# Performance work log

Measured on AMD Instinct MI355X. Metric: run time of the kernel, lower is better.

## Reference

```python
import jax, jax.numpy as jnp
import numpy as np
import math

VOCAB = 32000
D_MODEL = 512
N_LAYERS = 6
N_HEADS = 8
DIM_FF = 2048
B, L = 4, 2048
MAX_LEN = 5000
EPS = 1e-5


def _pos_encoding(max_len, d_model):
    pe = np.zeros((max_len, d_model), dtype=np.float32)
    pos = np.arange(max_len)[:, None].astype(np.float32)
    div = np.exp(np.arange(0, d_model, 2).astype(np.float32) * (-math.log(10000.0) / d_model))
    pe[:, 0::2] = np.sin(pos * div)
    pe[:, 1::2] = np.cos(pos * div)
    return jnp.asarray(pe)


def setup_inputs() -> dict:
    key = jax.random.key(0)
    ks = jax.random.split(key, 16)
    s = 0.02
    d, f, Ly = D_MODEL, DIM_FF, N_LAYERS
    inp = {
        "src": jax.random.randint(ks[0], (B, L), 0, VOCAB, dtype=jnp.int32),
        "embed": jax.random.normal(ks[1], (VOCAB, d), jnp.float32) * s,
        "pe": _pos_encoding(MAX_LEN, d),
        "Wq": jax.random.normal(ks[2], (Ly, d, d), jnp.float32) * s,
        "bq": jnp.zeros((Ly, d), jnp.float32),
        "Wk": jax.random.normal(ks[3], (Ly, d, d), jnp.float32) * s,
        "bk": jnp.zeros((Ly, d), jnp.float32),
        "Wv": jax.random.normal(ks[4], (Ly, d, d), jnp.float32) * s,
        "bv": jnp.zeros((Ly, d), jnp.float32),
        "Wo": jax.random.normal(ks[5], (Ly, d, d), jnp.float32) * s,
        "bo": jnp.zeros((Ly, d), jnp.float32),
        "W1": jax.random.normal(ks[6], (Ly, d, f), jnp.float32) * s,
        "b1": jnp.zeros((Ly, f), jnp.float32),
        "W2": jax.random.normal(ks[7], (Ly, f, d), jnp.float32) * s,
        "b2": jnp.zeros((Ly, d), jnp.float32),
        "g1": jnp.ones((Ly, d), jnp.float32),
        "be1": jnp.zeros((Ly, d), jnp.float32),
        "g2": jnp.ones((Ly, d), jnp.float32),
        "be2": jnp.zeros((Ly, d), jnp.float32),
    }
    return inp


def _layernorm(x, g, b):
    mu = jnp.mean(x, axis=-1, keepdims=True)
    var = jnp.mean((x - mu) ** 2, axis=-1, keepdims=True)
    return (x - mu) * jax.lax.rsqrt(var + EPS) * g + b


def _encoder(src, embed, pe, Wq, bq, Wk, bk, Wv, bv, Wo, bo, W1, b1, W2, b2, g1, be1, g2, be2):
    Bb, Ll = src.shape
    H = N_HEADS
    hd = D_MODEL // H
    x = embed[src] + pe[:Ll]  # [B, L, D]
    for i in range(Wq.shape[0]):
        # NOTE: faithful to the source: .view(B, H, L, hd) with NO transpose
        q = (x @ Wq[i] + bq[i]).reshape(Bb, H, Ll, hd)
        k = (x @ Wk[i] + bk[i]).reshape(Bb, H, Ll, hd)
        v = (x @ Wv[i] + bv[i]).reshape(Bb, H, Ll, hd)
        scores = jnp.einsum('bhqd,bhkd->bhqk', q, k) / math.sqrt(hd)
        w = jax.nn.softmax(scores, axis=-1)
        o = jnp.einsum('bhqk,bhkd->bhqd', w, v)
        o = o.transpose(0, 2, 1, 3).reshape(Bb, Ll, D_MODEL)
        o = o @ Wo[i] + bo[i]
        x = _layernorm(x + o, g1[i], be1[i])
        ff = jax.nn.relu(x @ W1[i] + b1[i]) @ W2[i] + b2[i]
        x = _layernorm(x + ff, g2[i], be2[i])
    return x


def reference(src, embed, pe, Wq, bq, Wk, bk, Wv, bv, Wo, bo, W1, b1, W2, b2, g1, be1, g2, be2):
    return _encoder(src, embed, pe, Wq, bq, Wk, bk, Wv, bv, Wo, bo, W1, b1, W2, b2, g1, be1, g2, be2)
```

## Files before the change

### kernel.cpp

```cpp
#include <hip/hip_runtime.h>
#include <hip/hip_bf16.h>

typedef unsigned short u16;
typedef __attribute__((ext_vector_type(8))) short bf16x8;
typedef __attribute__((ext_vector_type(2))) unsigned u32x2;
typedef __attribute__((ext_vector_type(4))) float f32x4;

#define B_  4
#define L_  2048
#define D_  512
#define H_  8
#define HD_ 64
#define FF_ 2048
#define NL_ 6
#define M_  8192
#define MB_ 1048576ULL

#if __has_builtin(__builtin_amdgcn_exp2f)
#define EX2 __builtin_amdgcn_exp2f
#else
#define EX2 exp2f
#endif

__device__ __forceinline__ float b2f(u16 u) {
    unsigned v = ((unsigned)u) << 16;
    return __builtin_bit_cast(float, v);
}
__device__ __forceinline__ u16 f2b(float f) {
    unsigned u = __builtin_bit_cast(unsigned, f);
    unsigned r = u + 0x7FFFu + ((u >> 16) & 1u);
    return (u16)(r >> 16);
}
__device__ __forceinline__ unsigned pack2_bf16(float a, float b) {
    __hip_bfloat162 h = __float22bfloat162_rn(make_float2(a, b));
    unsigned u;
    __builtin_memcpy(&u, &h, 4);
    return u;
}
__device__ __forceinline__ float inp(const void* p, size_t i, int fp32) {
    return fp32 ? ((const float*)p)[i] : b2f(((const u16*)p)[i]);
}
__device__ __forceinline__ void gl2lds16(const void* g, void* l) {
    __builtin_amdgcn_global_load_lds(
        (const __attribute__((address_space(1))) void*)g,
        (__attribute__((address_space(3))) void*)l, 16, 0, 0);
}

__global__ void probe_k(const unsigned* __restrict__ g1, int* __restrict__ flag) {
    flag[0] = (g1[0] == 0x3F800000u) ? 1 : 0;
}

__global__ __launch_bounds__(256) void transpose_layer_k2(const void* __restrict__ Wq,
                                                          const void* __restrict__ Wk,
                                                          const void* __restrict__ Wv,
                                                          const void* __restrict__ Wo,
                                                          const void* __restrict__ W1,
                                                          const void* __restrict__ W2,
                                                          size_t wo, size_t wf,
                                                          u16* __restrict__ Wt,
                                                          const int* __restrict__ flag) {
    __shared__ u16 tile[32][33];
    int fp32 = flag[0];
    int bid = blockIdx.x;
    const void* in;
    size_t off;
    u16* out;
    int rows, cols, tx, ty;
    if (bid < 1024) {
        int which = bid >> 8;
        in = (which == 0) ? Wq : (which == 1) ? Wk : (which == 2) ? Wv : Wo;
        off = wo;
        out = Wt + (size_t)which * (512 * 512);
        rows = 512; cols = 512;
        int t = bid & 255; tx = t & 15; ty = t >> 4;
    } else if (bid < 2048) {
        in = W1; off = wf; out = Wt + 4 * (512 * 512);
        rows = 512; cols = 2048;
        int t = bid - 1024; tx = t & 63; ty = t >> 6;
    } else {
        in = W2; off = wf; out = Wt + 4 * (512 * 512) + 512 * 2048;
        rows = 2048; cols = 512;
        int t = bid - 2048; tx = t & 15; ty = t >> 4;
    }
    int c0 = tx * 32, r0 = ty * 32;
    int lx = threadIdx.x & 31, ly = threadIdx.x >> 5;
    #pragma unroll
    for (int i = ly; i < 32; i += 8)
        tile[i][lx] = f2b(inp(in, off + (size_t)(r0 + i) * cols + c0 + lx, fp32));
    __syncthreads();
    #pragma unroll
    for (int i = ly; i < 32; i += 8)
        out[(size_t)(c0 + i) * rows + r0 + lx] = tile[lx][i];
}

__global__ __launch_bounds__(256) void embed_k(const int* __restrict__ src,
                                               const void* __restrict__ embed,
                                               const void* __restrict__ pe,
                                               float* __restrict__ xf,
                                               u16* __restrict__ xb,
                                               const int* __restrict__ flag) {
    int fp32 = flag[0];
    int idx = blockIdx.x * 256 + threadIdx.x;
    int m = idx >> 9;
    int d = idx & 511;
    int tok = src[m];
    float v = inp(embed, (size_t)tok * D_ + d, fp32)
            + inp(pe, (size_t)(m & (L_ - 1)) * D_ + d, fp32);
    xf[idx] = v;
    xb[idx] = f2b(v);
}

template <int TM, int TN, int WM, int WN, int WRITE_BF16, int RELU>
__device__ __forceinline__ void gemm_core(const u16* __restrict__ A,
                                          const u16* __restrict__ Bt,
                                          int tnB, int tnC,
                                          const void* __restrict__ bias, size_t boff,
                                          float* __restrict__ Cf, u16* __restrict__ Cb,
                                          int N, int K, int kbeg, int kend,
                                          float cscale, int fp32, int use_bias) {
    constexpr int BK = 32;
    __shared__ u16 Asm[TM * BK];
    __shared__ u16 Bsm[TN * BK];
    int tm = blockIdx.y * TM;
    int tid = threadIdx.x;
    int wave = tid >> 6, lane = tid & 63, quad = lane >> 4, l16 = lane & 15;
    constexpr int NWN = TN / WN;
    int wm = (wave / NWN) * WM, wn = (wave % NWN) * WN;
    constexpr int FI = WM / 16, FJ = WN / 16;
    constexpr int CA = TM / 64;
    constexpr int CB = TN / 64;

    int arowl = (lane >> 2);
    int akc   = (lane & 3) * 8;

    f32x4 acc[FI][FJ];
    #pragma unroll
    for (int i = 0; i < FI; i++)
        #pragma unroll
        for (int j = 0; j < FJ; j++) { f32x4 z = {0.f, 0.f, 0.f, 0.f}; acc[i][j] = z; }

    for (int k0 = kbeg; k0 < kend; k0 += BK) {
        __syncthreads();
        #pragma unroll
        for (int c = 0; c < CA; c++) {
            int chunk = wave * CA + c;
            int row = chunk * 16 + arowl;
            gl2lds16(A + (size_t)(tm + row) * K + k0 + akc, &Asm[chunk * 16 * BK]);
        }
        #pragma unroll
        for (int c = 0; c < CB; c++) {
            int chunk = wave * CB + c;
            int row = chunk * 16 + arowl;
            gl2lds16(Bt + (size_t)(tnB + row) * K + k0 + akc, &Bsm[chunk * 16 * BK]);
        }
        __syncthreads();
        bf16x8 af[FI], bfr[FJ];
        #pragma unroll
        for (int i = 0; i < FI; i++)
            af[i] = *(bf16x8*)&Asm[(wm + i * 16 + l16) * BK + quad * 8];
        #pragma unroll
        for (int j = 0; j < FJ; j++)
            bfr[j] = *(bf16x8*)&Bsm[(wn + j * 16 + l16) * BK + quad * 8];
        #pragma unroll
        for (int i = 0; i < FI; i++)
            #pragma unroll
            for (int j = 0; j < FJ; j++)
                acc[i][j] = __builtin_amdgcn_mfma_f32_16x16x32_bf16(af[i], bfr[j], acc[i][j], 0, 0, 0);
    }

    #pragma unroll
    for (int i = 0; i < FI; i++) {
        int row = tm + wm + i * 16 + quad * 4;
        #pragma unroll
        for (int j = 0; j < FJ; j++) {
            int col = tnC + wn + j * 16 + l16;
            float bv = use_bias ? inp(bias, boff + col, fp32) : 0.f;
            #pragma unroll
            for (int r = 0; r < 4; r++) {
                float v = (acc[i][j][r] + bv) * cscale;
                if (RELU) v = v > 0.f ? v : 0.f;
                size_t idx = (size_t)(row + r) * N + col;
                if (WRITE_BF16) Cb[idx] = f2b(v);
                else            Cf[idx] = v;
            }
        }
    }
}

__global__ __launch_bounds__(256) void gemm_qkv(const u16* A, const u16* Wt,
                                                const void* bq, const void* bk, const void* bv,
                                                size_t boff, u16* Qb, u16* Kb, u16* Vb,
                                                int K, float qscale, const int* flag) {
    int tnB = blockIdx.x * 128;
    int mat = tnB >> 9;
    int tnC = tnB & 511;
    u16* Cb = (mat == 0) ? Qb : (mat == 1) ? Kb : Vb;
    const void* bias = (mat == 0) ? bq : (mat == 1) ? bk : bv;
    float sc = (mat == 0) ? qscale : 1.0f;
    gemm_core<128, 128, 64, 64, 1, 0>(A, Wt, tnB, tnC, bias, boff, nullptr, Cb, 512, K, 0, K, sc, flag[0], 1);
}
__global__ __launch_bounds__(256) void gemm128_b16_relu(const u16* A, const u16* Bt, const void* bias, size_t boff,
                                                        u16* Cb, int N, int K, const int* flag) {
    int tn = blockIdx.x * 128;
    gemm_core<128, 128, 64, 64, 1, 1>(A, Bt, tn, tn, bias, boff, nullptr, Cb, N, K, 0, K, 1.0f, flag[0], 1);
}
__global__ __launch_bounds__(256) void gemm64_f32_sk(const u16* A, const u16* Bt, const void* bias, size_t boff,
                                                     float* Cf, int N, int K, const int* flag) {
    int tn = blockIdx.x * 128;
    int z = blockIdx.z;
    int ks = K / gridDim.z;
    gemm_core<64, 128, 64, 32, 0, 0>(A, Bt, tn, tn, bias, boff, Cf + (size_t)z * M_ * 512, nullptr,
                                     N, K, z * ks, z * ks + ks, 1.0f, flag[0], z == 0);
}

__global__ __launch_bounds__(256) void vperm_k(const u16* __restrict__ in, u16* __restrict__ out) {
    __shared__ u16 tile[32][33];
    int bh = blockIdx.z;
    const u16* pin = in + (size_t)bh * (L_ * HD_);
    u16* pout = out + (size_t)bh * (L_ * HD_);
    int c0 = blockIdx.x * 32, r0 = blockIdx.y * 32;
    int lx = threadIdx.x & 31, ly = threadIdx.x >> 5;
    #pragma unroll
    for (int i = ly; i < 32; i += 8)
        tile[i][lx] = pin[(size_t)(r0 + i) * HD_ + c0 + lx];
    __syncthreads();
    #pragma unroll
    for (int i = ly; i < 32; i += 8) {
        int k = r0 + lx;
        int kg = (k & ~63) | (((k & 15) << 2) | ((k >> 4) & 3));
        pout[(size_t)(c0 + i) * L_ + kg] = tile[lx][i];
    }
}

__global__ __launch_bounds__(256) void attn_k(const u16* __restrict__ Q,
                                              const u16* __restrict__ K,
                                              const u16* __restrict__ Vt,
                                              u16* __restrict__ O) {
    constexpr int LD = 72;
    __shared__ u16 Qs[64 * LD];
    __shared__ u16 Ks[64 * LD];
    __shared__ u16 Vs[64 * LD];
    int qt = blockIdx.x;
    int bh = blockIdx.y;
    int b = bh >> 3, h = bh & 7;
    size_t hb = (size_t)bh * (L_ * HD_);
    int tid = threadIdx.x, wave = tid >> 6, lane = tid & 63, quad = lane >> 4, l16 = lane & 15;

    #pragma unroll
    for (int s = 0; s < 2; s++) {
        int v = tid + s * 256;
        int row = v >> 3, col = (v & 7) * 8;
        *(bf16x8*)&Qs[row * LD + col] = *(const bf16x8*)(Q + hb + (size_t)(qt * 64 + row) * HD_ + col);
    }
    __syncthreads();
    bf16x8 aq0 = *(bf16x8*)&Qs[(wave * 16 + l16) * LD + quad * 8];
    bf16x8 aq1 = *(bf16x8*)&Qs[(wave * 16 + l16) * LD + 32 + quad * 8];
    __syncthreads();

    bf16x8 vones;
    #pragma unroll
    for (int i = 0; i < 8; i++) vones[i] = (short)0x3F80;

    f32x4 o[4];
    #pragma unroll
    for (int t = 0; t < 4; t++) { f32x4 z = {0.f, 0.f, 0.f, 0.f}; o[t] = z; }
    f32x4 lacc = {0.f, 0.f, 0.f, 0.f};

    for (int kt = 0; kt < L_ / 64; kt++) {
        __syncthreads();
        #pragma unroll
        for (int s = 0; s < 2; s++) {
            int v = tid + s * 256;
            int row = v >> 3, col = (v & 7) * 8;
            *(bf16x8*)&Ks[row * LD + col] = *(const bf16x8*)(K + hb + (size_t)(kt * 64 + row) * HD_ + col);
            *(bf16x8*)&Vs[row * LD + col] = *(const bf16x8*)(Vt + hb + (size_t)row * L_ + kt * 64 + col);
        }
        __syncthreads();

        f32x4 s4[4];
        #pragma unroll
        for (int t = 0; t < 4; t++) {
            f32x4 z = {0.f, 0.f, 0.f, 0.f};
            bf16x8 bk0 = *(bf16x8*)&Ks[(t * 16 + l16) * LD + quad * 8];
            bf16x8 bk1 = *(bf16x8*)&Ks[(t * 16 + l16) * LD + 32 + quad * 8];
            z = __builtin_amdgcn_mfma_f32_16x16x32_bf16(aq0, bk0, z, 0, 0, 0);
            z = __builtin_amdgcn_mfma_f32_16x16x32_bf16(aq1, bk1, z, 0, 0, 0);
            s4[t] = z;
        }

        #pragma unroll
        for (int r = 0; r < 4; r++) {
            float p0 = EX2(s4[0][r]);
            float p1 = EX2(s4[1][r]);
            float p2 = EX2(s4[2][r]);
            float p3 = EX2(s4[3][r]);
            u32x2 pk;
            pk[0] = pack2_bf16(p0, p1);
            pk[1] = pack2_bf16(p2, p3);
            *(u32x2*)&Qs[(wave * 16 + quad * 4 + r) * LD + l16 * 4] = pk;
        }
        #pragma unroll
        for (int ks = 0; ks < 2; ks++) {
            bf16x8 ap = *(bf16x8*)&Qs[(wave * 16 + l16) * LD + ks * 32 + quad * 8];
            #pragma unroll
            for (int t = 0; t < 4; t++) {
                bf16x8 bv = *(bf16x8*)&Vs[(t * 16 + l16) * LD + ks * 32 + quad * 8];
                o[t] = __builtin_amdgcn_mfma_f32_16x16x32_bf16(ap, bv, o[t], 0, 0, 0);
            }
            lacc = __builtin_amdgcn_mfma_f32_16x16x32_bf16(ap, vones, lacc, 0, 0, 0);
        }
    }

    float linv[4];
    #pragma unroll
    for (int r = 0; r < 4; r++) linv[r] = 1.0f / fmaxf(lacc[r], 1e-30f);
    #pragma unroll
    for (int t = 0; t < 4; t++)
        #pragma unroll
        for (int r = 0; r < 4; r++) {
            float v = o[t][r] * linv[r];
            int l2 = qt * 64 + wave * 16 + quad * 4 + r;
            O[((size_t)b * L_ + l2) * D_ + h * HD_ + t * 16 + l16] = f2b(v);
        }
}

__global__ __launch_bounds__(256) void ln_k2(const float* resid,
                                             const float* __restrict__ delta0,
                                             const float* __restrict__ delta1,
                                             const void* __restrict__ g,
                                             const void* __restrict__ be, size_t goff,
                                             float* xf_out,
                                             void* __restrict__ out_raw,
                                             const int* __restrict__ flag,
                                             int two, int is_final) {
    int fp32 = flag[0];
    int row = blockIdx.x * 4 + (threadIdx.x >> 6);
    int lane = threadIdx.x & 63;
    const float* pr = resid + (size_t)row * D_;
    const float* pd0 = delta0 + (size_t)row * D_;
    const float* pd1 = delta1 + (size_t)row * D_;
    float u[8];
    float s = 0.f;
    #pragma unroll
    for (int i = 0; i < 8; i++) {
        int c = lane + i * 64;
        u[i] = pr[c] + pd0[c] + (two ? pd1[c] : 0.f);
        s += u[i];
    }
    #pragma unroll
    for (int d = 1; d < 64; d <<= 1) s += __shfl_xor(s, d);
    float mu = s * (1.0f / 512.0f);
    float vs = 0.f;
    #pragma unroll
    for (int i = 0; i < 8; i++) { float t = u[i] - mu; vs += t * t; }
    #pragma unroll
    for (int d = 1; d < 64; d <<= 1) vs += __shfl_xor(vs, d);
    float rstd = rsqrtf(vs * (1.0f / 512.0f) + 1e-5f);
    #pragma unroll
    for (int i = 0; i < 8; i++) {
        int c = lane + i * 64;
        float v = (u[i] - mu) * rstd * inp(g, goff + c, fp32) + inp(be, goff + c, fp32);
        xf_out[(size_t)row * D_ + c] = v;
        size_t oi = (size_t)row * D_ + c;
        if (is_final && fp32) ((float*)out_raw)[oi] = v;
        else                  ((u16*)out_raw)[oi]  = f2b(v);
    }
}

extern "C" void kernel_launch(void* const* d_in, const int* in_sizes, int n_in,
                              void* d_out, int out_size, void* d_ws, size_t ws_size,
                              hipStream_t stream) {
    (void)in_sizes; (void)n_in; (void)out_size;
    const int*  src   = (const int*)d_in[0];
    const void* embed = d_in[1];
    const void* pe    = d_in[2];
    const void* Wq = d_in[3];  const void* bq = d_in[4];
    const void* Wk = d_in[5];  const void* bk = d_in[6];
    const void* Wv = d_in[7];  const void* bv = d_in[8];
    const void* Wo = d_in[9];  const void* bo = d_in[10];
    const void* W1 = d_in[11]; const void* b1 = d_in[12];
    const void* W2 = d_in[13]; const void* b2 = d_in[14];
    const void* g1 = d_in[15]; const void* be1 = d_in[16];
    const void* g2 = d_in[17]; const void* be2 = d_in[18];

    int big = (ws_size >= 103 * MB_ + 64);
    char* ws = (char*)d_ws;
    float* xf  = (float*)(ws);
    u16*  xb   = (u16*)(ws + 16 * MB_);
    u16*  Qb   = (u16*)(ws + 24 * MB_);
    u16*  Kb   = (u16*)(ws + 32 * MB_);
    u16*  Vb   = (u16*)(ws + 40 * MB_);
    u16*  Vt   = (u16*)(ws + 48 * MB_);
    u16*  Ab   = (u16*)(ws + 56 * MB_);
    float* Pf0 = (float*)(ws + 24 * MB_);
    float* Pf1 = (float*)(ws + 40 * MB_);
    u16*  Hb   = (u16*)(ws + (big ? 64 : 40) * MB_);
    u16*  Wt   = (u16*)(ws + (big ? 96 : 72) * MB_);
    int*  flag = (int*)(ws + (big ? 102 : 78) * MB_);
    u16* Wot = Wt + 786432;
    u16* W1t = Wt + 1048576;
    u16* W2t = Wt + 2097152;

    const float QSCALE = 0.125f * 1.44269504f;

    probe_k<<<1, 1, 0, stream>>>((const unsigned*)g1, flag);
    embed_k<<<(M_ * D_) / 256, 256, 0, stream>>>(src, embed, pe, xf, xb, flag);

    for (int i = 0; i < NL_; i++) {
        size_t wo = (size_t)i * 512 * 512;
        size_t wf = (size_t)i * 512 * 2048;
        size_t vo = (size_t)i * 512;
        size_t fo = (size_t)i * 2048;
        transpose_layer_k2<<<3072, 256, 0, stream>>>(Wq, Wk, Wv, Wo, W1, W2, wo, wf, Wt, flag);

        gemm_qkv<<<dim3(12, 64), 256, 0, stream>>>(xb, Wt, bq, bk, bv, vo, Qb, Kb, Vb, 512, QSCALE, flag);
        vperm_k<<<dim3(2, 64, 32), 256, 0, stream>>>(Vb, Vt);
        attn_k<<<dim3(32, 32), 256, 0, stream>>>(Qb, Kb, Vt, Ab);
        gemm64_f32_sk<<<dim3(4, 128, 2), 256, 0, stream>>>(Ab, Wot, bo, vo, Pf0, 512, 512, flag);
        ln_k2<<<M_ / 4, 256, 0, stream>>>(xf, Pf0, Pf1, g1, be1, vo, xf, xb, flag, 1, 0);
        gemm128_b16_relu<<<dim3(16, 64), 256, 0, stream>>>(xb, W1t, b1, fo, Hb, 2048, 512, flag);
        if (big) gemm64_f32_sk<<<dim3(4, 128, 2), 256, 0, stream>>>(Hb, W2t, b2, vo, Pf0, 512, 2048, flag);
        else     gemm64_f32_sk<<<dim3(4, 128, 1), 256, 0, stream>>>(Hb, W2t, b2, vo, Pf0, 512, 2048, flag);
        void* out_raw = (i == NL_ - 1) ? d_out : (void*)xb;
        ln_k2<<<M_ / 4, 256, 0, stream>>>(xf, Pf0, Pf1, g2, be2, vo, xf, out_raw, flag, big ? 1 : 0, (i == NL_ - 1) ? 1 : 0);
    }
}
```

Measured before the change: 1.465 ms.

## Rework attention kernel with 32x32 MFMA tiles and register-prefetched K/V

Attention now uses 32x32x16 MFMAs with four waves split 2x2 over query rows and key/head columns. It prefetches the next K/V tile into registers while computing the current one, and replaces __syncthreads with a plain lgkmcnt wait plus barrier. The V permutation in vperm_k is dropped to match the new P-tile layout, and the row-sum is reduced through shared memory. The aim is fewer MFMA issues and hidden global-load latency, at the cost of more registers, extra barriers, and scalar bf16 stores for P.

```diff
diff --git a/kernel.cpp b/kernel.cpp
--- a/kernel.cpp
+++ b/kernel.cpp
@@ -5,6 +5,7 @@
 typedef __attribute__((ext_vector_type(8))) short bf16x8;
 typedef __attribute__((ext_vector_type(2))) unsigned u32x2;
 typedef __attribute__((ext_vector_type(4))) float f32x4;
+typedef __attribute__((ext_vector_type(16))) float f32x16;
 
 #define B_  4
 #define L_  2048
@@ -44,6 +45,10 @@
     __builtin_amdgcn_global_load_lds(
         (const __attribute__((address_space(1))) void*)g,
         (__attribute__((address_space(3))) void*)l, 16, 0, 0);
+}
+__device__ __forceinline__ void bar_lds() {
+    asm volatile("s_waitcnt lgkmcnt(0)" ::: "memory");
+    __builtin_amdgcn_s_barrier();
 }
 
 __global__ void probe_k(const unsigned* __restrict__ g1, int* __restrict__ flag) {
@@ -225,11 +230,8 @@
         tile[i][lx] = pin[(size_t)(r0 + i) * HD_ + c0 + lx];
     __syncthreads();
     #pragma unroll
-    for (int i = ly; i < 32; i += 8) {
-        int k = r0 + lx;
-        int kg = (k & ~63) | (((k & 15) << 2) | ((k >> 4) & 3));
-        pout[(size_t)(c0 + i) * L_ + kg] = tile[lx][i];
-    }
+    for (int i = ly; i < 32; i += 8)
+        pout[(size_t)(c0 + i) * L_ + r0 + lx] = tile[lx][i];
 }
 
 __global__ __launch_bounds__(256) void attn_k(const u16* __restrict__ Q,
@@ -237,91 +239,110 @@
                                               const u16* __restrict__ Vt,
                                               u16* __restrict__ O) {
     constexpr int LD = 72;
-    __shared__ u16 Qs[64 * LD];
+    constexpr int NT = L_ / 64;
     __shared__ u16 Ks[64 * LD];
     __shared__ u16 Vs[64 * LD];
+    __shared__ u16 Ps[64 * LD];
+    __shared__ float Ls[64];
     int qt = blockIdx.x;
     int bh = blockIdx.y;
     int b = bh >> 3, h = bh & 7;
     size_t hb = (size_t)bh * (L_ * HD_);
-    int tid = threadIdx.x, wave = tid >> 6, lane = tid & 63, quad = lane >> 4, l16 = lane & 15;
-
+    int tid = threadIdx.x;
+    int wave = tid >> 6, lane = tid & 63, hi = lane >> 5, r32 = lane & 31;
+    int wq = wave >> 1, wc = wave & 1;
+
+    int srow[2], scol[2];
+    #pragma unroll
+    for (int s = 0; s < 2; s++) { int v = tid + s * 256; srow[s] = v >> 3; scol[s] = (v & 7) * 8; }
+
+    bf16x8 kreg[2], vreg[2];
     #pragma unroll
     for (int s = 0; s < 2; s++) {
-        int v = tid + s * 256;
-        int row = v >> 3, col = (v & 7) * 8;
-        *(bf16x8*)&Qs[row * LD + col] = *(const bf16x8*)(Q + hb + (size_t)(qt * 64 + row) * HD_ + col);
-    }
-    __syncthreads();
-    bf16x8 aq0 = *(bf16x8*)&Qs[(wave * 16 + l16) * LD + quad * 8];
-    bf16x8 aq1 = *(bf16x8*)&Qs[(wave * 16 + l16) * LD + 32 + quad * 8];
-    __syncthreads();
+        kreg[s] = *(const bf16x8*)(K + hb + (size_t)srow[s] * HD_ + scol[s]);
+        vreg[s] = *(const bf16x8*)(Vt + hb + (size_t)srow[s] * L_ + scol[s]);
+    }
+
+    #pragma unroll
+    for (int s = 0; s < 2; s++)
+        *(bf16x8*)&Ps[srow[s] * LD + scol[s]] =
+            *(const bf16x8*)(Q + hb + (size_t)(qt * 64 + srow[s]) * HD_ + scol[s]);
+    bar_lds();
+    bf16x8 aq[4];
+    #pragma unroll
+    for (int dc = 0; dc < 4; dc++)
+        aq[dc] = *(bf16x8*)&Ps[(wq * 32 + r32) * LD + dc * 16 + hi * 8];
+    bar_lds();
 
     bf16x8 vones;
     #pragma unroll
     for (int i = 0; i < 8; i++) vones[i] = (short)0x3F80;
 
-    f32x4 o[4];
-    #pragma unroll
-    for (int t = 0; t < 4; t++) { f32x4 z = {0.f, 0.f, 0.f, 0.f}; o[t] = z; }
-    f32x4 lacc = {0.f, 0.f, 0.f, 0.f};
-
-    for (int kt = 0; kt < L_ / 64; kt++) {
-        __syncthreads();
+    f32x16 oac, lac;
+    #pragma unroll
+    for (int i = 0; i < 16; i++) { oac[i] = 0.f; lac[i] = 0.f; }
+
+    for (int kt = 0; kt < NT; kt++) {
         #pragma unroll
         for (int s = 0; s < 2; s++) {
-            int v = tid + s * 256;
-            int row = v >> 3, col = (v & 7) * 8;
-            *(bf16x8*)&Ks[row * LD + col] = *(const bf16x8*)(K + hb + (size_t)(kt * 64 + row) * HD_ + col);
-            *(bf16x8*)&Vs[row * LD + col] = *(const bf16x8*)(Vt + hb + (size_t)row * L_ + kt * 64 + col);
-        }
-        __syncthreads();
-
-        f32x4 s4[4];
-        #pragma unroll
-        for (int t = 0; t < 4; t++) {
-            f32x4 z = {0.f, 0.f, 0.f, 0.f};
-            bf16x8 bk0 = *(bf16x8*)&Ks[(t * 16 + l16) * LD + quad * 8];
-            bf16x8 bk1 = *(bf16x8*)&Ks[(t * 16 + l16) * LD + 32 + quad * 8];
-            z = __builtin_amdgcn_mfma_f32_16x16x32_bf16(aq0, bk0, z, 0, 0, 0);
-            z = __builtin_amdgcn_mfma_f32_16x16x32_bf16(aq1, bk1, z, 0, 0, 0);
-            s4[t] = z;
-        }
-
-        #pragma unroll
-        for (int r = 0; r < 4; r++) {
-            float p0 = EX2(s4[0][r]);
-            float p1 = EX2(s4[1][r]);
-            float p2 = EX2(s4[2][r]);
-            float p3 = EX2(s4[3][r]);
-            u32x2 pk;
-            pk[0] = pack2_bf16(p0, p1);
-            pk[1] = pack2_bf16(p2, p3);
-            *(u32x2*)&Qs[(wave * 16 + quad * 4 + r) * LD + l16 * 4] = pk;
-        }
-        #pragma unroll
-        for (int ks = 0; ks < 2; ks++) {
-            bf16x8 ap = *(bf16x8*)&Qs[(wave * 16 + l16) * LD + ks * 32 + quad * 8];
+            *(bf16x8*)&Ks[srow[s] * LD + scol[s]] = kreg[s];
+            *(bf16x8*)&Vs[srow[s] * LD + scol[s]] = vreg[s];
+        }
+        bar_lds();
+        if (kt + 1 < NT) {
             #pragma unroll
-            for (int t = 0; t < 4; t++) {
-                bf16x8 bv = *(bf16x8*)&Vs[(t * 16 + l16) * LD + ks * 32 + quad * 8];
-                o[t] = __builtin_amdgcn_mfma_f32_16x16x32_bf16(ap, bv, o[t], 0, 0, 0);
+            for (int s = 0; s < 2; s++) {
+                kreg[s] = *(const bf16x8*)(K + hb + (size_t)((kt + 1) * 64 + srow[s]) * HD_ + scol[s]);
+                vreg[s] = *(const bf16x8*)(Vt + hb + (size_t)srow[s] * L_ + (kt + 1) * 64 + scol[s]);
             }
-            lacc = __builtin_amdgcn_mfma_f32_16x16x32_bf16(ap, vones, lacc, 0, 0, 0);
-        }
-    }
-
-    float linv[4];
-    #pragma unroll
-    for (int r = 0; r < 4; r++) linv[r] = 1.0f / fmaxf(lacc[r], 1e-30f);
-    #pragma unroll
-    for (int t = 0; t < 4; t++)
-        #pragma unroll
-        for (int r = 0; r < 4; r++) {
-            float v = o[t][r] * linv[r];
-            int l2 = qt * 64 + wave * 16 + quad * 4 + r;
-            O[((size_t)b * L_ + l2) * D_ + h * HD_ + t * 16 + l16] = f2b(v);
-        }
+        }
+
+        f32x16 sac;
+        #pragma unroll
+        for (int i = 0; i < 16; i++) sac[i] = 0.f;
+        __builtin_amdgcn_s_setprio(1);
+        #pragma unroll
+        for (int dc = 0; dc < 4; dc++) {
+            bf16x8 bk = *(bf16x8*)&Ks[(wc * 32 + r32) * LD + dc * 16 + hi * 8];
+            sac = __builtin_amdgcn_mfma_f32_32x32x16_bf16(aq[dc], bk, sac, 0, 0, 0);
+        }
+        __builtin_amdgcn_s_setprio(0);
+
+        int pbase = (wq * 32 + 4 * hi) * LD + wc * 32 + r32;
+        #pragma unroll
+        for (int r = 0; r < 16; r++) {
+            float p = EX2(sac[r]);
+            Ps[pbase + ((r & 3) + 8 * (r >> 2)) * LD] = f2b(p);
+        }
+        bar_lds();
+
+        __builtin_amdgcn_s_setprio(1);
+        #pragma unroll
+        for (int kc = 0; kc < 4; kc++) {
+            bf16x8 ap = *(bf16x8*)&Ps[(wq * 32 + r32) * LD + kc * 16 + hi * 8];
+            bf16x8 bv = *(bf16x8*)&Vs[(wc * 32 + r32) * LD + kc * 16 + hi * 8];
+            oac = __builtin_amdgcn_mfma_f32_32x32x16_bf16(ap, bv, oac, 0, 0, 0);
+            if (wc == 0)
+                lac = __builtin_amdgcn_mfma_f32_32x32x16_bf16(ap, vones, lac, 0, 0, 0);
+        }
+        __builtin_amdgcn_s_setprio(0);
+        bar_lds();
+    }
+
+    if (wc == 0 && r32 == 0) {
+        #pragma unroll
+        for (int r = 0; r < 16; r++)
+            Ls[wq * 32 + 4 * hi + (r & 3) + 8 * (r >> 2)] = lac[r];
+    }
+    bar_lds();
+
+    #pragma unroll
+    for (int r = 0; r < 16; r++) {
+        int row = wq * 32 + 4 * hi + (r & 3) + 8 * (r >> 2);
+        float v = oac[r] * (1.0f / fmaxf(Ls[row], 1e-30f));
+        int l2 = qt * 64 + row;
+        O[((size_t)b * L_ + l2) * D_ + h * HD_ + wc * 32 + r32] = f2b(v);
+    }
 }
 
 __global__ __launch_bounds__(256) void ln_k2(const float* resid,
```

New measurement: 1.520 ms. 3.8% more time.
